# Optimization experiments

Hardware: AMD Instinct MI355X
Metric: run time of the kernel (lower is better)

## Reference

```python
import jax, jax.numpy as jnp
import numpy as np

B_SZ, SEQ_LEN, STATE_DIM, D_IN, D_OUT, KX = 8, 2048, 1024, 512, 512, 10


def setup_inputs() -> dict:
    key = jax.random.key(0)
    ks = jax.random.split(key, 7)
    inputs = jax.random.normal(ks[0], (B_SZ, SEQ_LEN, D_IN), dtype=jnp.float32)
    h0 = jax.random.normal(ks[1], (STATE_DIM,), dtype=jnp.float32)
    # exponential_decay_init(lam=15): x = clamp(-1/lam * log(1-u), max=1); A = (1-x)*sign
    u = jax.random.uniform(ks[2], (STATE_DIM,), dtype=jnp.float32)
    x = jnp.minimum(-(1.0 / 15.0) * jnp.log1p(-u), 1.0)
    sign = jnp.sign(jax.random.normal(ks[3], (STATE_DIM,), dtype=jnp.float32))
    A = (1.0 - x) * sign
    Bm = jax.random.normal(ks[4], (D_IN, STATE_DIM), dtype=jnp.float32) / D_IN
    C = jax.random.normal(ks[5], (STATE_DIM, D_OUT), dtype=jnp.float32) / STATE_DIM
    M = jax.random.normal(ks[6], (D_OUT, D_IN, KX), dtype=jnp.float32) / D_OUT
    return {"inputs": inputs, "h0": h0, "A": A, "B": Bm, "C": C, "M": M}


def _ar_preds(M, x):
    # Equivalent to einsum('oik,bli->bklo') + per-k roll + triu mask + sum over k:
    # ar[b,l,:] = sum_{i=0}^{k-1, i<=l} M[:,:,i] @ x[b, l-i, :]
    b, l, d_in = x.shape
    kx = M.shape[2]
    ar = jnp.einsum('oi,bli->blo', M[:, :, 0], x)
    for i in range(1, kx):
        x_shift = jnp.pad(x, ((0, 0), (i, 0), (0, 0)))[:, :l]  # shift right, zero-fill
        ar = ar + jnp.einsum('oi,bli->blo', M[:, :, i], x_shift)
    return ar


def reference(inputs, h0, A, B, C, M):
    b, l, d_in = inputs.shape
    state_dim = A.shape[0]
    # Project inputs once: u_t @ B for all t -> [b, l, s]
    uB = jnp.einsum('bli,is->bls', inputs, B)

    def step(h, u_t):
        h = A * h + u_t  # diagonal recurrence
        return h, h

    h_init = jnp.broadcast_to(h0, (b, state_dim))
    _, hs = jax.lax.scan(step, h_init, jnp.swapaxes(uB, 0, 1))  # [l, b, s]
    hs = jnp.swapaxes(hs, 0, 1)  # [b, l, s]
    lds_out = hs @ C  # [b, l, d_out]
    return lds_out + _ar_preds(M, inputs)
```

## Files before the change

kernel.cpp:

```cpp
#include <hip/hip_runtime.h>

#define B_SZ   8
#define SEQ    2048
#define PSEQ   (SEQ+16)
#define SDIM   1024
#define DIN    512
#define DOUT   512
#define KX     10
#define RTOT   (B_SZ*SEQ)
#define LC     64
#define NC     (SEQ/LC)

typedef __attribute__((ext_vector_type(8))) short short8;
typedef __attribute__((ext_vector_type(4))) float f32x4;
typedef __attribute__((ext_vector_type(4))) unsigned short bfx4;

#define OFF_XP   0UL
#define OFF_UB   16908288UL
#define OFF_HS   50462720UL
#define OFF_BT   84017152UL
#define OFF_CT   85065728UL
#define OFF_MT   86114304UL

__device__ __forceinline__ short f2bf(float f) {
  unsigned u = __builtin_bit_cast(unsigned, f);
  u += 0x7fffu + ((u >> 16) & 1u);
  return (short)(u >> 16);
}
__device__ __forceinline__ float bf2f(unsigned short b) {
  return __builtin_bit_cast(float, (unsigned)b << 16);
}

#define GLOAD16(gp, lp) __builtin_amdgcn_global_load_lds( \
    (const __attribute__((address_space(1))) void*)(gp), \
    (__attribute__((address_space(3))) void*)(lp), 16, 0, 0)

__global__ void k_conv_x(const float* __restrict__ in, short* __restrict__ out) {
  const int NG = RTOT * (DIN / 8);
  for (int g = blockIdx.x * 256 + threadIdx.x; g < NG; g += 2048 * 256) {
    int r = g >> 6, c8 = g & 63;
    int b = r >> 11, t = r & 2047;
    const float4* p = reinterpret_cast<const float4*>(in) + (size_t)g * 2;
    float4 f0 = p[0], f1 = p[1];
    short8 o;
    o[0]=f2bf(f0.x); o[1]=f2bf(f0.y); o[2]=f2bf(f0.z); o[3]=f2bf(f0.w);
    o[4]=f2bf(f1.x); o[5]=f2bf(f1.y); o[6]=f2bf(f1.z); o[7]=f2bf(f1.w);
    *reinterpret_cast<short8*>(out + ((size_t)(b * PSEQ + 16 + t) * DIN + c8 * 8)) = o;
  }
}

__global__ void k_zero_pad(short* __restrict__ Xp) {
  int idx = blockIdx.x * 256 + threadIdx.x;
  if (idx >= B_SZ * 16 * (DIN / 8)) return;
  int b = idx >> 10, rem = idx & 1023;
  int row16 = rem >> 6, c8 = rem & 63;
  const short8 z = {0,0,0,0,0,0,0,0};
  *reinterpret_cast<short8*>(Xp + ((size_t)(b * PSEQ + row16) * DIN + c8 * 8)) = z;
}

__global__ void k_transpose_bf16(const float* __restrict__ in, short* __restrict__ out,
                                 int rows, int cols) {
  __shared__ float t[32][33];
  int bx = blockIdx.x * 32, by = blockIdx.y * 32;
  int tx = threadIdx.x & 31, ty = threadIdx.x >> 5;
  #pragma unroll
  for (int j = 0; j < 32; j += 8)
    t[ty + j][tx] = in[(size_t)(by + ty + j) * cols + (bx + tx)];
  __syncthreads();
  #pragma unroll
  for (int j = 0; j < 32; j += 8)
    out[(size_t)(bx + ty + j) * rows + (by + tx)] = f2bf(t[tx][ty + j]);
}

__global__ void k_prep_M(const float* __restrict__ M, short* __restrict__ Mt) {
  int idx = blockIdx.x * 256 + threadIdx.x;
  if (idx >= DOUT * DIN) return;
  int o = idx / DIN, i = idx - o * DIN;
  const float* src = M + ((size_t)o * DIN + i) * KX;
  #pragma unroll
  for (int t = 0; t < KX; ++t)
    Mt[((size_t)t * DOUT + o) * DIN + i] = f2bf(src[t]);
}

__global__ void k_scan_E(const short* __restrict__ uB, const float* __restrict__ A,
                         float* __restrict__ E) {
  int blk = blockIdx.x, tid = threadIdx.x;
  int b = blk >> 5, c = blk & 31;
  int s0 = tid * 4;
  const short* base = uB + ((size_t)b * SEQ + (size_t)c * LC) * SDIM + s0;
  float a[4], h[4];
  #pragma unroll
  for (int j = 0; j < 4; ++j) { a[j] = A[s0 + j]; h[j] = 0.f; }
  for (int t = 0; t < LC; ++t) {
    bfx4 v = *reinterpret_cast<const bfx4*>(base + (size_t)t * SDIM);
    #pragma unroll
    for (int j = 0; j < 4; ++j) h[j] = fmaf(a[j], h[j], bf2f(v[j]));
  }
  float* ep = E + (size_t)blk * SDIM + s0;
  #pragma unroll
  for (int j = 0; j < 4; ++j) ep[j] = h[j];
}

__global__ void k_scan_S(const float* __restrict__ E, const float* __restrict__ A,
                         const float* __restrict__ h0, float* __restrict__ Sb) {
  int blk = blockIdx.x, tid = threadIdx.x;
  int b = blk >> 2;
  int s = ((blk & 3) << 8) + tid;
  float a = A[s], ap = a;
  #pragma unroll
  for (int q = 0; q < 6; ++q) ap *= ap;
  float S = h0[s];
  for (int c = 0; c < NC; ++c) {
    size_t idx = ((size_t)b * NC + c) * SDIM + s;
    Sb[idx] = S;
    S = fmaf(ap, S, E[idx]);
  }
}

__global__ void k_scan_h(const short* __restrict__ uB, const float* __restrict__ A,
                         const float* __restrict__ Sb, short* __restrict__ hs) {
  int blk = blockIdx.x, tid = threadIdx.x;
  int b = blk >> 5, c = blk & 31;
  int s0 = tid * 4;
  const short* base = uB + ((size_t)b * SEQ + (size_t)c * LC) * SDIM + s0;
  short* hbase = hs + ((size_t)b * SEQ + (size_t)c * LC) * SDIM + s0;
  float a[4], h[4];
  #pragma unroll
  for (int j = 0; j < 4; ++j) {
    a[j] = A[s0 + j];
    h[j] = Sb[(size_t)blk * SDIM + s0 + j];
  }
  for (int t = 0; t < LC; ++t) {
    bfx4 v = *reinterpret_cast<const bfx4*>(base + (size_t)t * SDIM);
    bfx4 o;
    #pragma unroll
    for (int j = 0; j < 4; ++j) {
      h[j] = fmaf(a[j], h[j], bf2f(v[j]));
      o[j] = (unsigned short)f2bf(h[j]);
    }
    *reinterpret_cast<bfx4*>(hbase + (size_t)t * SDIM) = o;
  }
}


__device__ __forceinline__ void stage32(const short* __restrict__ g0, int ld,
                                        short* l0, int w, int lane) {
  int r8 = lane >> 3;
  int slot = (lane & 7) ^ r8;
  const char* gb = (const char*)g0 + slot * 16;
  #pragma unroll
  for (int i = 0; i < 4; ++i) {
    int row = w * 32 + i * 8;
    GLOAD16(gb + ((size_t)(row + r8) * ld) * 2, l0 + row * 64);
  }
}

__device__ __forceinline__ void mfma_Ktile_swz(const short* lA, const short* lB,
                                               int lane, int wm, int wn, f32x4 acc[4][4]) {
  int lr = lane & 15;
  int h  = lane >> 4;
  #pragma unroll
  for (int kk = 0; kk < 64; kk += 32) {
    int kslot = (kk >> 3) + h;
    short8 af[4], bfr[4];
    #pragma unroll
    for (int mi = 0; mi < 4; ++mi) {
      int row = wm * 64 + mi * 16 + lr;
      af[mi] = *reinterpret_cast<const short8*>(lA + row * 64 + ((kslot ^ (row & 7)) << 3));
    }
    #pragma unroll
    for (int ni = 0; ni < 4; ++ni) {
      int row = wn * 64 + ni * 16 + lr;
      bfr[ni] = *reinterpret_cast<const short8*>(lB + row * 64 + ((kslot ^ (row & 7)) << 3));
    }
    #pragma unroll
    for (int mi = 0; mi < 4; ++mi)
      #pragma unroll
      for (int ni = 0; ni < 4; ++ni)
        acc[mi][ni] = __builtin_amdgcn_mfma_f32_16x16x32_bf16(af[mi], bfr[ni], acc[mi][ni], 0, 0, 0);
  }
}

__global__ __launch_bounds__(256) void k_gemm_uB(const short* __restrict__ Xp,
                                                 const short* __restrict__ Bt,
                                                 short* __restrict__ uB) {
  __shared__ __attribute__((aligned(16))) short lA[128 * 64];
  __shared__ __attribute__((aligned(16))) short lB[128 * 64];
  int tid = threadIdx.x, lane = tid & 63, w = tid >> 6, wm = w >> 1, wn = w & 1;
  long r0 = (long)blockIdx.x * 128;
  int  c0 = blockIdx.y * 128;
  int  b  = (int)(r0 >> 11);
  const short* Abase = Xp + (size_t)(r0 + 16 * (b + 1)) * DIN;
  const f32x4 z4 = {0.f, 0.f, 0.f, 0.f};
  f32x4 acc[4][4];
  #pragma unroll
  for (int mi = 0; mi < 4; ++mi)
    #pragma unroll
    for (int ni = 0; ni < 4; ++ni) acc[mi][ni] = z4;

  for (int k0 = 0; k0 < DIN; k0 += 64) {
    stage32(Abase + k0, DIN, lA, w, lane);
    stage32(Bt + (size_t)c0 * DIN + k0, DIN, lB, w, lane);
    __syncthreads();
    mfma_Ktile_swz(lA, lB, lane, wm, wn, acc);
    __syncthreads();
  }
  #pragma unroll
  for (int mi = 0; mi < 4; ++mi)
    #pragma unroll
    for (int ni = 0; ni < 4; ++ni)
      #pragma unroll
      for (int r = 0; r < 4; ++r) {
        long row = r0 + wm * 64 + mi * 16 + (lane >> 4) * 4 + r;
        int  col = c0 + wn * 64 + ni * 16 + (lane & 15);
        uB[(size_t)row * SDIM + col] = f2bf(acc[mi][ni][r]);
      }
}

__global__ __launch_bounds__(256) void k_gemm_out(const short* __restrict__ hs,
                                                  const short* __restrict__ Xp,
                                                  const short* __restrict__ Ct,
                                                  const short* __restrict__ Mt,
                                                  float* __restrict__ out) {
  __shared__ __attribute__((aligned(16))) short lA[128 * 64];
  __shared__ __attribute__((aligned(16))) short lB[128 * 64];
  int tid = threadIdx.x, lane = tid & 63, w = tid >> 6, wm = w >> 1, wn = w & 1;
  long r0 = (long)blockIdx.x * 128;
  int  c0 = blockIdx.y * 128;
  int  b  = (int)(r0 >> 11);
  const f32x4 z4 = {0.f, 0.f, 0.f, 0.f};
  f32x4 acc[4][4];
  #pragma unroll
  for (int mi = 0; mi < 4; ++mi)
    #pragma unroll
    for (int ni = 0; ni < 4; ++ni) acc[mi][ni] = z4;

  for (int k0 = 0; k0 < SDIM; k0 += 64) {
    stage32(hs + (size_t)r0 * SDIM + k0, SDIM, lA, w, lane);
    stage32(Ct + (size_t)c0 * SDIM + k0, SDIM, lB, w, lane);
    __syncthreads();
    mfma_Ktile_swz(lA, lB, lane, wm, wn, acc);
    __syncthreads();
  }
  for (int tap = 0; tap < KX; ++tap) {
    const short* Abase = Xp + (size_t)(r0 + 16 * (b + 1) - tap) * DIN;
    const short* Bbase = Mt + (size_t)tap * DOUT * DIN + (size_t)c0 * DIN;
    for (int k0 = 0; k0 < DIN; k0 += 64) {
      stage32(Abase + k0, DIN, lA, w, lane);
      stage32(Bbase + k0, DIN, lB, w, lane);
      __syncthreads();
      mfma_Ktile_swz(lA, lB, lane, wm, wn, acc);
      __syncthreads();
    }
  }
  #pragma unroll
  for (int mi = 0; mi < 4; ++mi)
    #pragma unroll
    for (int ni = 0; ni < 4; ++ni)
      #pragma unroll
      for (int r = 0; r < 4; ++r) {
        long row = r0 + wm * 64 + mi * 16 + (lane >> 4) * 4 + r;
        int  col = c0 + wn * 64 + ni * 16 + (lane & 15);
        out[(size_t)row * DOUT + col] = acc[mi][ni][r];
      }
}

extern "C" void kernel_launch(void* const* d_in, const int* in_sizes, int n_in,
                              void* d_out, int out_size, void* d_ws, size_t ws_size,
                              hipStream_t stream) {
  (void)in_sizes; (void)n_in; (void)out_size; (void)ws_size;
  const float* x  = (const float*)d_in[0];
  const float* h0 = (const float*)d_in[1];
  const float* A  = (const float*)d_in[2];
  const float* B  = (const float*)d_in[3];
  const float* C  = (const float*)d_in[4];
  const float* M  = (const float*)d_in[5];
  float* out = (float*)d_out;
  char* ws = (char*)d_ws;

  short* Xp  = (short*)(ws + OFF_XP);
  short* uB  = (short*)(ws + OFF_UB);
  short* hsb = (short*)(ws + OFF_HS);
  short* Bt  = (short*)(ws + OFF_BT);
  short* Ct  = (short*)(ws + OFF_CT);
  short* Mt  = (short*)(ws + OFF_MT);
  float* E   = out;
  float* Sb  = out + B_SZ * NC * SDIM;

  k_conv_x<<<2048, 256, 0, stream>>>(x, Xp);
  k_zero_pad<<<32, 256, 0, stream>>>(Xp);
  k_transpose_bf16<<<dim3(SDIM / 32, DIN / 32), 256, 0, stream>>>(B, Bt, DIN, SDIM);
  k_transpose_bf16<<<dim3(DOUT / 32, SDIM / 32), 256, 0, stream>>>(C, Ct, SDIM, DOUT);
  k_prep_M<<<(DOUT * DIN + 255) / 256, 256, 0, stream>>>(M, Mt);

  k_gemm_uB<<<dim3(RTOT / 128, SDIM / 128), 256, 0, stream>>>(Xp, Bt, uB);

  k_scan_E<<<B_SZ * NC, 256, 0, stream>>>(uB, A, E);
  k_scan_S<<<B_SZ * 4, 256, 0, stream>>>(E, A, h0, Sb);
  k_scan_h<<<B_SZ * NC, 256, 0, stream>>>(uB, A, Sb, hsb);

  k_gemm_out<<<dim3(RTOT / 128, DOUT / 128), 256, 0, stream>>>(hsb, Xp, Ct, Mt, out);
}
```

Before: 178.4 us.

## Double-buffer output GEMM with 256x128 tiles, 512 threads and swizzled block order

Rewrites the fused output GEMM (hs@C plus the AR taps) as one 96-step K loop. Each step prefetches the tile two steps ahead into double-buffered LDS, waiting with vmcnt instead of syncing around every stage. Block tiles grow to 256x128 with 8 waves, the grid becomes 256 blocks with a remapped block order for L2 locality, and MFMA issue is bracketed with setprio. The aim is to hide global load latency behind MFMA work and to reuse the B tile across more rows, at the cost of more LDS per block and fewer blocks per CU.

New measurement: 187.6 us. 1.05x slower.

```diff
diff --git a/kernel.cpp b/kernel.cpp
--- a/kernel.cpp
+++ b/kernel.cpp
@@ -141,7 +141,6 @@
     *reinterpret_cast<bfx4*>(hbase + (size_t)t * SDIM) = o;
   }
 }
-
 
 __device__ __forceinline__ void stage32(const short* __restrict__ g0, int ld,
                                         short* l0, int w, int lane) {
@@ -217,17 +216,92 @@
       }
 }
 
-__global__ __launch_bounds__(256) void k_gemm_out(const short* __restrict__ hs,
+#define NKT   96
+#define ABUF  (256 * 64)
+#define BBUF  (128 * 64)
+#define BUFSZ (ABUF + BBUF)
+
+__device__ __forceinline__ void tile_ptrs(int kt, long r0, int c0, int b,
+                                          const short* __restrict__ hs,
+                                          const short* __restrict__ Xp,
+                                          const short* __restrict__ Ct,
+                                          const short* __restrict__ Mt,
+                                          const short** pA, const short** pB, int* ld) {
+  if (kt < 16) {
+    *pA = hs + (size_t)r0 * SDIM + kt * 64;
+    *pB = Ct + (size_t)c0 * SDIM + kt * 64;
+    *ld = SDIM;
+  } else {
+    int t = kt - 16;
+    int tap = t >> 3;
+    int k0 = (t & 7) * 64;
+    *pA = Xp + (size_t)(r0 + 16 * (b + 1) - tap) * DIN + k0;
+    *pB = Mt + (size_t)tap * DOUT * DIN + (size_t)c0 * DIN + k0;
+    *ld = DIN;
+  }
+}
+
+__device__ __forceinline__ void stage_tile(const short* __restrict__ pA,
+                                           const short* __restrict__ pB, int ld,
+                                           short* buf, int tid) {
+  int rsub = tid >> 3;
+  int slot = (tid & 7) ^ (rsub & 7);
+  short* la = buf;
+  short* lb = buf + ABUF;
+  #pragma unroll
+  for (int i = 0; i < 4; ++i) {
+    int row = i * 64 + rsub;
+    GLOAD16(pA + (size_t)row * ld + slot * 8, la + row * 64 + (tid & 7) * 8);
+  }
+  #pragma unroll
+  for (int i = 0; i < 2; ++i) {
+    int row = i * 64 + rsub;
+    GLOAD16(pB + (size_t)row * ld + slot * 8, lb + row * 64 + (tid & 7) * 8);
+  }
+}
+
+__device__ __forceinline__ void compute_tile(const short* la, const short* lb,
+                                             int lane, int wm, int wn, f32x4 acc[4][4]) {
+  int lr = lane & 15;
+  int h  = lane >> 4;
+  #pragma unroll
+  for (int kk = 0; kk < 64; kk += 32) {
+    int kslot = (kk >> 3) + h;
+    short8 af[4], bfr[4];
+    #pragma unroll
+    for (int mi = 0; mi < 4; ++mi) {
+      int row = wm * 64 + mi * 16 + lr;
+      af[mi] = *reinterpret_cast<const short8*>(la + row * 64 + ((kslot ^ (row & 7)) << 3));
+    }
+    #pragma unroll
+    for (int ni = 0; ni < 4; ++ni) {
+      int row = wn * 64 + ni * 16 + lr;
+      bfr[ni] = *reinterpret_cast<const short8*>(lb + row * 64 + ((kslot ^ (row & 7)) << 3));
+    }
+    __builtin_amdgcn_s_setprio(1);
+    #pragma unroll
+    for (int mi = 0; mi < 4; ++mi)
+      #pragma unroll
+      for (int ni = 0; ni < 4; ++ni)
+        acc[mi][ni] = __builtin_amdgcn_mfma_f32_16x16x32_bf16(af[mi], bfr[ni], acc[mi][ni], 0, 0, 0);
+    __builtin_amdgcn_s_setprio(0);
+  }
+}
+
+__global__ __launch_bounds__(512) void k_gemm_out(const short* __restrict__ hs,
                                                   const short* __restrict__ Xp,
                                                   const short* __restrict__ Ct,
                                                   const short* __restrict__ Mt,
                                                   float* __restrict__ out) {
-  __shared__ __attribute__((aligned(16))) short lA[128 * 64];
-  __shared__ __attribute__((aligned(16))) short lB[128 * 64];
-  int tid = threadIdx.x, lane = tid & 63, w = tid >> 6, wm = w >> 1, wn = w & 1;
-  long r0 = (long)blockIdx.x * 128;
-  int  c0 = blockIdx.y * 128;
+  __shared__ __attribute__((aligned(16))) short lds[2][BUFSZ];
+  int tid = threadIdx.x, lane = tid & 63, w = tid >> 6;
+  int wm = w >> 1, wn = w & 1;
+  int bid = blockIdx.x;
+  int sw  = (bid & 7) * 32 + (bid >> 3);
+  long r0 = (long)(sw & 63) * 256;
+  int  c0 = (sw >> 6) * 128;
   int  b  = (int)(r0 >> 11);
+
   const f32x4 z4 = {0.f, 0.f, 0.f, 0.f};
   f32x4 acc[4][4];
   #pragma unroll
@@ -235,24 +309,28 @@
     #pragma unroll
     for (int ni = 0; ni < 4; ++ni) acc[mi][ni] = z4;
 
-  for (int k0 = 0; k0 < SDIM; k0 += 64) {
-    stage32(hs + (size_t)r0 * SDIM + k0, SDIM, lA, w, lane);
-    stage32(Ct + (size_t)c0 * SDIM + k0, SDIM, lB, w, lane);
-    __syncthreads();
-    mfma_Ktile_swz(lA, lB, lane, wm, wn, acc);
-    __syncthreads();
-  }
-  for (int tap = 0; tap < KX; ++tap) {
-    const short* Abase = Xp + (size_t)(r0 + 16 * (b + 1) - tap) * DIN;
-    const short* Bbase = Mt + (size_t)tap * DOUT * DIN + (size_t)c0 * DIN;
-    for (int k0 = 0; k0 < DIN; k0 += 64) {
-      stage32(Abase + k0, DIN, lA, w, lane);
-      stage32(Bbase + k0, DIN, lB, w, lane);
-      __syncthreads();
-      mfma_Ktile_swz(lA, lB, lane, wm, wn, acc);
-      __syncthreads();
-    }
-  }
+  const short *pA, *pB; int ld;
+  tile_ptrs(0, r0, c0, b, hs, Xp, Ct, Mt, &pA, &pB, &ld);
+  stage_tile(pA, pB, ld, lds[0], tid);
+  tile_ptrs(1, r0, c0, b, hs, Xp, Ct, Mt, &pA, &pB, &ld);
+  stage_tile(pA, pB, ld, lds[1], tid);
+  asm volatile("s_waitcnt vmcnt(6)" ::: "memory");
+  __builtin_amdgcn_s_barrier();
+
+  for (int kt = 0; kt < NKT; ++kt) {
+    short* cur = lds[kt & 1];
+    compute_tile(cur, cur + ABUF, lane, wm, wn, acc);
+    __builtin_amdgcn_s_barrier();
+    if (kt + 2 < NKT) {
+      tile_ptrs(kt + 2, r0, c0, b, hs, Xp, Ct, Mt, &pA, &pB, &ld);
+      stage_tile(pA, pB, ld, cur, tid);
+      asm volatile("s_waitcnt vmcnt(6)" ::: "memory");
+    } else {
+      asm volatile("s_waitcnt vmcnt(0)" ::: "memory");
+    }
+    __builtin_amdgcn_s_barrier();
+  }
+
   #pragma unroll
   for (int mi = 0; mi < 4; ++mi)
     #pragma unroll
@@ -299,5 +377,5 @@
   k_scan_S<<<B_SZ * 4, 256, 0, stream>>>(E, A, h0, Sb);
   k_scan_h<<<B_SZ * NC, 256, 0, stream>>>(uB, A, Sb, hsb);
 
-  k_gemm_out<<<dim3(RTOT / 128, DOUT / 128), 256, 0, stream>>>(hsb, Xp, Ct, Mt, out);
-}
+  k_gemm_out<<<256, 512, 0, stream>>>(hsb, Xp, Ct, Mt, out);
+}
```

## Double-buffer GEMM K-loops and reuse one staged X tile across all AR taps

Applied to the files above, without the earlier changes.

Both GEMM kernels now prefetch the next K-tile into a second LDS buffer with global_load_lds. They wait on partial vmcnt counts instead of fencing every tile with two full syncthreads. In the output kernel, the autoregressive part stages a single 144-row X slab per K chunk and reuses it for all 10 taps by offsetting rows, so only the M tiles are streamed and double-buffered. MFMA sections are also wrapped in s_setprio. LDS use per block doubles to 64 KB, which may limit occupancy, and the hand-counted vmcnt waits must match the number of loads issued.

Result: faster. 156.0 us (-12.6%).

```diff
diff --git a/kernel.cpp b/kernel.cpp
--- a/kernel.cpp
+++ b/kernel.cpp
@@ -34,6 +34,8 @@
 #define GLOAD16(gp, lp) __builtin_amdgcn_global_load_lds( \
     (const __attribute__((address_space(1))) void*)(gp), \
     (__attribute__((address_space(3))) void*)(lp), 16, 0, 0)
+#define WAITVM(n) asm volatile("s_waitcnt vmcnt(" #n ")" ::: "memory")
+#define SBAR() __builtin_amdgcn_s_barrier()
 
 __global__ void k_conv_x(const float* __restrict__ in, short* __restrict__ out) {
   const int NG = RTOT * (DIN / 8);
@@ -142,30 +144,38 @@
   }
 }
 
-
-__device__ __forceinline__ void stage32(const short* __restrict__ g0, int ld,
-                                        short* l0, int w, int lane) {
-  int r8 = lane >> 3;
-  int slot = (lane & 7) ^ r8;
-  const char* gb = (const char*)g0 + slot * 16;
+__device__ __forceinline__ void stage128(const short* __restrict__ g, int ld,
+                                         short* l, int tid) {
+  int rsub = tid >> 3;
+  int slot = (tid & 7) ^ (rsub & 7);
   #pragma unroll
   for (int i = 0; i < 4; ++i) {
-    int row = w * 32 + i * 8;
-    GLOAD16(gb + ((size_t)(row + r8) * ld) * 2, l0 + row * 64);
-  }
-}
-
-__device__ __forceinline__ void mfma_Ktile_swz(const short* lA, const short* lB,
-                                               int lane, int wm, int wn, f32x4 acc[4][4]) {
+    int row = i * 32 + rsub;
+    GLOAD16(g + (size_t)row * ld + slot * 8, l + row * 64 + (tid & 7) * 8);
+  }
+}
+__device__ __forceinline__ void stage144(const short* __restrict__ g, int ld,
+                                         short* l, int tid) {
+  stage128(g, ld, l, tid);
+  if (tid < 128) {
+    int rsub = tid >> 3;
+    int slot = (tid & 7) ^ (rsub & 7);
+    int row = 128 + rsub;
+    GLOAD16(g + (size_t)row * ld + slot * 8, l + row * 64 + (tid & 7) * 8);
+  }
+}
+
+__device__ __forceinline__ void mfma_tile(const short* lA, int aoff, const short* lB,
+                                          int lane, int wm, int wn, f32x4 acc[4][4]) {
   int lr = lane & 15;
   int h  = lane >> 4;
   #pragma unroll
-  for (int kk = 0; kk < 64; kk += 32) {
-    int kslot = (kk >> 3) + h;
+  for (int kk = 0; kk < 2; ++kk) {
+    int kslot = kk * 4 + h;
     short8 af[4], bfr[4];
     #pragma unroll
     for (int mi = 0; mi < 4; ++mi) {
-      int row = wm * 64 + mi * 16 + lr;
+      int row = aoff + wm * 64 + mi * 16 + lr;
       af[mi] = *reinterpret_cast<const short8*>(lA + row * 64 + ((kslot ^ (row & 7)) << 3));
     }
     #pragma unroll
@@ -173,24 +183,28 @@
       int row = wn * 64 + ni * 16 + lr;
       bfr[ni] = *reinterpret_cast<const short8*>(lB + row * 64 + ((kslot ^ (row & 7)) << 3));
     }
+    __builtin_amdgcn_s_setprio(1);
     #pragma unroll
     for (int mi = 0; mi < 4; ++mi)
       #pragma unroll
       for (int ni = 0; ni < 4; ++ni)
         acc[mi][ni] = __builtin_amdgcn_mfma_f32_16x16x32_bf16(af[mi], bfr[ni], acc[mi][ni], 0, 0, 0);
+    __builtin_amdgcn_s_setprio(0);
   }
 }
 
 __global__ __launch_bounds__(256) void k_gemm_uB(const short* __restrict__ Xp,
                                                  const short* __restrict__ Bt,
                                                  short* __restrict__ uB) {
-  __shared__ __attribute__((aligned(16))) short lA[128 * 64];
-  __shared__ __attribute__((aligned(16))) short lB[128 * 64];
+  __shared__ __attribute__((aligned(16))) short lds[32768];
+  short* A0 = lds;         short* B0 = lds + 8192;
+  short* A1 = lds + 16384; short* B1 = lds + 24576;
   int tid = threadIdx.x, lane = tid & 63, w = tid >> 6, wm = w >> 1, wn = w & 1;
   long r0 = (long)blockIdx.x * 128;
   int  c0 = blockIdx.y * 128;
   int  b  = (int)(r0 >> 11);
   const short* Abase = Xp + (size_t)(r0 + 16 * (b + 1)) * DIN;
+  const short* Bbase = Bt + (size_t)c0 * DIN;
   const f32x4 z4 = {0.f, 0.f, 0.f, 0.f};
   f32x4 acc[4][4];
   #pragma unroll
@@ -198,12 +212,25 @@
     #pragma unroll
     for (int ni = 0; ni < 4; ++ni) acc[mi][ni] = z4;
 
-  for (int k0 = 0; k0 < DIN; k0 += 64) {
-    stage32(Abase + k0, DIN, lA, w, lane);
-    stage32(Bt + (size_t)c0 * DIN + k0, DIN, lB, w, lane);
-    __syncthreads();
-    mfma_Ktile_swz(lA, lB, lane, wm, wn, acc);
-    __syncthreads();
+  stage128(Abase, DIN, A0, tid);      stage128(Bbase, DIN, B0, tid);
+  stage128(Abase + 64, DIN, A1, tid); stage128(Bbase + 64, DIN, B1, tid);
+  WAITVM(8);
+  SBAR();
+  for (int kt = 0; kt < 8; ++kt) {
+    const short* a  = (kt & 1) ? A1 : A0;
+    const short* bb = (kt & 1) ? B1 : B0;
+    mfma_tile(a, 0, bb, lane, wm, wn, acc);
+    SBAR();
+    if (kt + 2 < 8) {
+      short* ad = (kt & 1) ? A1 : A0;
+      short* bd = (kt & 1) ? B1 : B0;
+      stage128(Abase + (kt + 2) * 64, DIN, ad, tid);
+      stage128(Bbase + (kt + 2) * 64, DIN, bd, tid);
+      WAITVM(8);
+    } else {
+      WAITVM(0);
+    }
+    SBAR();
   }
   #pragma unroll
   for (int mi = 0; mi < 4; ++mi)
@@ -222,12 +249,19 @@
                                                   const short* __restrict__ Ct,
                                                   const short* __restrict__ Mt,
                                                   float* __restrict__ out) {
-  __shared__ __attribute__((aligned(16))) short lA[128 * 64];
-  __shared__ __attribute__((aligned(16))) short lB[128 * 64];
+  __shared__ __attribute__((aligned(16))) short lds[32768];
+  short* A0 = lds;         short* B0 = lds + 8192;
+  short* A1 = lds + 16384; short* B1 = lds + 24576;
+  short* Xs = lds;
+  short* M0 = lds + 16384;
+  short* M1 = lds + 24576;
   int tid = threadIdx.x, lane = tid & 63, w = tid >> 6, wm = w >> 1, wn = w & 1;
   long r0 = (long)blockIdx.x * 128;
   int  c0 = blockIdx.y * 128;
   int  b  = (int)(r0 >> 11);
+  const short* hsA = hs + (size_t)r0 * SDIM;
+  const short* CtB = Ct + (size_t)c0 * SDIM;
+  const short* Xa  = Xp + (size_t)(r0 + 16 * (b + 1) - 16) * DIN;
   const f32x4 z4 = {0.f, 0.f, 0.f, 0.f};
   f32x4 acc[4][4];
   #pragma unroll
@@ -235,24 +269,49 @@
     #pragma unroll
     for (int ni = 0; ni < 4; ++ni) acc[mi][ni] = z4;
 
-  for (int k0 = 0; k0 < SDIM; k0 += 64) {
-    stage32(hs + (size_t)r0 * SDIM + k0, SDIM, lA, w, lane);
-    stage32(Ct + (size_t)c0 * SDIM + k0, SDIM, lB, w, lane);
-    __syncthreads();
-    mfma_Ktile_swz(lA, lB, lane, wm, wn, acc);
-    __syncthreads();
-  }
-  for (int tap = 0; tap < KX; ++tap) {
-    const short* Abase = Xp + (size_t)(r0 + 16 * (b + 1) - tap) * DIN;
-    const short* Bbase = Mt + (size_t)tap * DOUT * DIN + (size_t)c0 * DIN;
-    for (int k0 = 0; k0 < DIN; k0 += 64) {
-      stage32(Abase + k0, DIN, lA, w, lane);
-      stage32(Bbase + k0, DIN, lB, w, lane);
-      __syncthreads();
-      mfma_Ktile_swz(lA, lB, lane, wm, wn, acc);
-      __syncthreads();
-    }
-  }
+  stage128(hsA, SDIM, A0, tid);      stage128(CtB, SDIM, B0, tid);
+  stage128(hsA + 64, SDIM, A1, tid); stage128(CtB + 64, SDIM, B1, tid);
+  WAITVM(8);
+  SBAR();
+  for (int kt = 0; kt < 16; ++kt) {
+    const short* a  = (kt & 1) ? A1 : A0;
+    const short* bb = (kt & 1) ? B1 : B0;
+    mfma_tile(a, 0, bb, lane, wm, wn, acc);
+    SBAR();
+    if (kt + 2 < 16) {
+      short* ad = (kt & 1) ? A1 : A0;
+      short* bd = (kt & 1) ? B1 : B0;
+      stage128(hsA + (kt + 2) * 64, SDIM, ad, tid);
+      stage128(CtB + (kt + 2) * 64, SDIM, bd, tid);
+      WAITVM(8);
+    } else {
+      WAITVM(0);
+    }
+    SBAR();
+  }
+
+  for (int k0 = 0; k0 < 8; ++k0) {
+    int kc = k0 * 64;
+    stage144(Xa + kc, DIN, Xs, tid);
+    stage128(Mt + (size_t)c0 * DIN + kc, DIN, M0, tid);
+    stage128(Mt + (size_t)DOUT * DIN + (size_t)c0 * DIN + kc, DIN, M1, tid);
+    WAITVM(4);
+    SBAR();
+    for (int tap = 0; tap < KX; ++tap) {
+      const short* mb = (tap & 1) ? M1 : M0;
+      mfma_tile(Xs, 16 - tap, mb, lane, wm, wn, acc);
+      SBAR();
+      if (tap + 2 < KX) {
+        short* md = (tap & 1) ? M1 : M0;
+        stage128(Mt + (size_t)(tap + 2) * DOUT * DIN + (size_t)c0 * DIN + kc, DIN, md, tid);
+        WAITVM(4);
+      } else {
+        WAITVM(0);
+      }
+      SBAR();
+    }
+  }
+
   #pragma unroll
   for (int mi = 0; mi < 4; ++mi)
     #pragma unroll
```
